# Kernel optimization log

Hardware: AMD Instinct MI355X
Metric: run time of the kernel (lower is better)

The kernel has to match this reference:

```python
import jax, jax.numpy as jnp
import numpy as np

H = 512      # hidden == embed (required: process-block LSTM consumes attention output of size hidden)
XY = 2
CITY_T = 100
BATCH = 512
INIT = 0.08  # uniform(-0.08, 0.08) weight init


def _unif(key, shape):
    return jax.random.uniform(key, shape, jnp.float32, minval=-INIT, maxval=INIT)


def lstm_cell(x, h, c, Wih, Whh, bih, bhh):
    # PyTorch gate order: i, f, g, o
    g = x @ Wih.T + h @ Whh.T + (bih + bhh)
    i, f, gg, o = jnp.split(g, 4, axis=-1)
    c_new = jax.nn.sigmoid(f) * c + jax.nn.sigmoid(i) * jnp.tanh(gg)
    h_new = jax.nn.sigmoid(o) * jnp.tanh(c_new)
    return h_new, c_new


def setup_inputs() -> dict:
    key = jax.random.key(0)
    ks = jax.random.split(key, 20)
    inp = {
        "x": jax.random.uniform(ks[0], (BATCH, CITY_T, XY), jnp.float32),      # city coords in [0,1)
        "dec_i1": jax.random.uniform(ks[1], (BATCH, H), jnp.float32),          # torch.rand(batch,1,hidden)
        "W_emb": _unif(ks[2], (H, XY)),
        "enc_Wih": _unif(ks[3], (4 * H, H)),
        "enc_Whh": _unif(ks[4], (4 * H, H)),
        "enc_bih": _unif(ks[5], (4 * H,)),
        "enc_bhh": _unif(ks[6], (4 * H,)),
        "dec_Wih": _unif(ks[7], (4 * H, H)),
        "dec_Whh": _unif(ks[8], (4 * H, H)),
        "dec_bih": _unif(ks[9], (4 * H,)),
        "dec_bhh": _unif(ks[10], (4 * H,)),
        "W_q": _unif(ks[11], (H, H)),
        "W_ref": _unif(ks[12], (H, H)),
        "v": _unif(ks[13], (1, H)),       # Vec: Linear(hidden,1,bias=False)
        "fc1": _unif(ks[14], (H, H)),
        "fc2": _unif(ks[15], (1, H)),
    }
    return inp


def reference(x, dec_i1, W_emb, enc_Wih, enc_Whh, enc_bih, enc_bhh,
              dec_Wih, dec_Whh, dec_bih, dec_bhh, W_q, W_ref, v, fc1, fc2):
    batch, city_t, _ = x.shape
    emb = x @ W_emb.T                                   # (b, c, H)

    # ---- Encoder LSTM (zero initial state) ----
    h0 = jnp.zeros((batch, H), emb.dtype)
    c0 = jnp.zeros((batch, H), emb.dtype)

    def enc_step(carry, xt):
        h, c = carry
        h, c = lstm_cell(xt, h, c, enc_Wih, enc_Whh, enc_bih, enc_bhh)
        return (h, c), h

    (hT, cT), enc_h = jax.lax.scan(enc_step, (h0, c0), jnp.swapaxes(emb, 0, 1))
    enc_h = jnp.swapaxes(enc_h, 0, 1)                   # (b, c, H)

    # W_ref(enc_h) is static across decode steps -> compute once
    u1 = enc_h @ W_ref.T                                # (b, c, H)

    # ---- Decoder: city_t steps of LSTM cell + Bahdanau attention ----
    def dec_step(carry, _):
        dec_i, h, c = carry
        h, c = lstm_cell(dec_i, h, c, dec_Wih, dec_Whh, dec_bih, dec_bhh)
        u2 = h @ W_q.T                                  # (b, H)
        u = jnp.tanh(u1 + u2[:, None, :]) @ v[0]        # (b, c)
        a = jax.nn.softmax(u, axis=1)
        d = jnp.einsum('bc,bch->bh', a, enc_h)          # glimpse (b, H)
        return (d, h, c), None

    (_, h_last, _), _ = jax.lax.scan(dec_step, (dec_i1, hT, cT), None, length=city_t)

    # final2FC: Linear->ReLU->Linear -> scalar per batch
    pred_l = jax.nn.relu(h_last @ fc1.T) @ fc2.T        # (b, 1)
    return pred_l[:, 0]
```

## Files before the change

### kernel.cpp

```cpp
#include <hip/hip_runtime.h>
#include <hip/hip_bf16.h>

#define H 512
#define TSTEPS 100
#define BATCH 512
#define KB 16
#define NBLK 256
#define NT 1024
#define NGRP 8
#define GBLK 32

typedef __attribute__((ext_vector_type(8))) short bf16x8;
typedef __attribute__((ext_vector_type(8))) unsigned short u16x8;
typedef __attribute__((ext_vector_type(4))) float f32x4;
typedef unsigned short u16;

__device__ __forceinline__ float bf2f(u16 u) {
    union { unsigned int i; float f; } z; z.i = ((unsigned int)u) << 16; return z.f;
}
__device__ __forceinline__ u16 f2bf(float f) {
    union { float f; unsigned int u; } z; z.f = f;
    unsigned int r = (z.u + 0x7fffu + ((z.u >> 16) & 1u)) >> 16;
    return (u16)r;
}
__device__ __forceinline__ float sigmoidf_(float x) { return 1.0f / (1.0f + __expf(-x)); }
__device__ __forceinline__ float ftanh(float x) {
    x = fminf(15.0f, fmaxf(-15.0f, x));
    float e = __expf(2.0f * x);
    return (e - 1.0f) / (e + 1.0f);
}
__device__ __forceinline__ f32x4 MF(bf16x8 a, bf16x8 b, f32x4 c) {
    return __builtin_amdgcn_mfma_f32_16x16x32_bf16(a, b, c, 0, 0, 0);
}

__device__ __forceinline__ size_t pidx(int m, int k) {
    int kb = k >> 5, kin = k & 31;
    int lane = (m & 15) + (((kin >> 2) & 3) << 4);
    int j = (kin & 3) + ((kin >> 4) << 2);
    return ((size_t)((m >> 4) * KB + kb) * 64 + lane) * 8 + j;
}

__device__ __forceinline__ void fbar(unsigned* flags, int grp, int bib, unsigned target) {
    __syncthreads();
    if (threadIdx.x < 64) {
        if (threadIdx.x == 0)
            __hip_atomic_store(&flags[(grp * 32 + bib) * 16], target,
                               __ATOMIC_RELEASE, __HIP_MEMORY_SCOPE_AGENT);
        const int l = threadIdx.x;
        bool done;
        do {
            unsigned v = target;
            if (l < 32)
                v = __hip_atomic_load(&flags[(grp * 32 + l) * 16],
                                      __ATOMIC_RELAXED, __HIP_MEMORY_SCOPE_AGENT);
            done = __all((int)(v >= target));
            if (!done) __builtin_amdgcn_s_sleep(1);
        } while (!done);
        __threadfence();
    }
    __syncthreads();
}

__global__ void prep_kernel(const float* __restrict__ W_emb, const float* __restrict__ enc_Wih,
                            const float* __restrict__ enc_bih, const float* __restrict__ enc_bhh,
                            const float* __restrict__ dec_bih, const float* __restrict__ dec_bhh,
                            float* __restrict__ Wc, float* __restrict__ bc, float* __restrict__ db) {
    int g = blockIdx.x * blockDim.x + threadIdx.x;
    if (g >= 4 * H) return;
    float s0 = 0.f, s1 = 0.f;
    for (int j = 0; j < H; ++j) {
        float w = enc_Wih[(size_t)g * H + j];
        s0 += w * W_emb[j * 2 + 0];
        s1 += w * W_emb[j * 2 + 1];
    }
    Wc[g * 2 + 0] = s0; Wc[g * 2 + 1] = s1;
    bc[g] = enc_bih[g] + enc_bhh[g];
    db[g] = dec_bih[g] + dec_bhh[g];
}

__global__ void pack_w(const float* __restrict__ W, u16* __restrict__ hi, u16* __restrict__ lo,
                       int total) {
    int idx = blockIdx.x * 256 + threadIdx.x;
    if (idx >= total) return;
    int m = idx >> 9, k = idx & 511;
    float v = W[idx];
    u16 h16 = f2bf(v);
    u16 l16 = f2bf(v - bf2f(h16));
    size_t p = pidx(m, k);
    hi[p] = h16; lo[p] = l16;
}

__global__ void zero4(float* __restrict__ p, int n) {
    int i = blockIdx.x * blockDim.x + threadIdx.x;
    if (i < n) p[i] = 0.f;
}

__global__ __launch_bounds__(NT, 1) void persist_enc(
    const float* __restrict__ x, const float* __restrict__ Wc, const float* __restrict__ bc,
    const u16* __restrict__ WeH, const u16* __restrict__ WeL,
    float* __restrict__ cbuf, u16* __restrict__ hbuf,
    u16* __restrict__ ench, unsigned* __restrict__ fE) {
    extern __shared__ char smem[];
    u16* wlds = (u16*)smem;
    float* exch = (float*)(smem + 131072);
    const int tid = threadIdx.x;
    const int lane = tid & 63;
    const int w = tid >> 6;
    const int q = w & 3, j = w >> 2;
    const int blk = blockIdx.x;
    const int grp = blk & 7, nni = blk >> 3;
    const size_t BHs = (size_t)BATCH * H;

    for (int c = 0; c < 8; ++c) {
        int cq = c >> 1, hl = c & 1;
        const u16x8* s8 = (const u16x8*)((hl ? WeL : WeH) + (size_t)((cq * 32 + nni) * KB) * 512);
        u16x8* d8 = (u16x8*)(wlds + c * 8192);
        for (int i = tid; i < 1024; i += NT) d8[i] = s8[i];
    }
    __syncthreads();

    for (int t = 0; t < TSTEPS; ++t) {
        const u16* Ah = hbuf + (size_t)(t & 1) * 2 * BHs;
        const u16* Al = Ah + BHs;
        u16* Hh = hbuf + (size_t)((t + 1) & 1) * 2 * BHs;
        u16* Hl = Hh + BHs;
        f32x4 acc = {};
#pragma unroll 4
        for (int kb = 0; kb < KB; ++kb) {
            bf16x8 bh = *(const bf16x8*)&wlds[((q * 2 + 0) * KB + kb) * 512 + lane * 8];
            bf16x8 bl = *(const bf16x8*)&wlds[((q * 2 + 1) * KB + kb) * 512 + lane * 8];
            size_t ab = ((size_t)((grp * 4 + j) * KB + kb) * 64 + lane) * 8;
            bf16x8 ah = *(const bf16x8*)&Ah[ab];
            bf16x8 al = *(const bf16x8*)&Al[ab];
            acc = MF(ah, bh, acc);
            acc = MF(ah, bl, acc);
            acc = MF(al, bh, acc);
        }
        const int col = lane & 15, rg = lane >> 4;
#pragma unroll
        for (int r = 0; r < 4; ++r)
            exch[(q * 64 + j * 16 + rg * 4 + r) * 16 + col] = acc[r];
        __syncthreads();
        {
            int lb = tid >> 4, cl = tid & 15;
            int b = grp * 64 + lb, n = nni * 16 + cl;
            float x0 = x[((size_t)b * TSTEPS + t) * 2 + 0];
            float x1 = x[((size_t)b * TSTEPS + t) * 2 + 1];
            float g[4];
#pragma unroll
            for (int qq = 0; qq < 4; ++qq)
                g[qq] = exch[(qq * 64 + lb) * 16 + cl] + bc[qq * H + n]
                      + x0 * Wc[(qq * H + n) * 2 + 0] + x1 * Wc[(qq * H + n) * 2 + 1];
            size_t ci = (size_t)b * H + n;
            float cn = sigmoidf_(g[1]) * cbuf[ci] + sigmoidf_(g[0]) * ftanh(g[2]);
            float hn = sigmoidf_(g[3]) * ftanh(cn);
            cbuf[ci] = cn;
            u16 hh = f2bf(hn), hl16 = f2bf(hn - bf2f(hh));
            size_t p = pidx(b, n);
            Hh[p] = hh; Hl[p] = hl16;
            ench[((size_t)b * TSTEPS + t) * H + n] = hh;
        }
        fbar(fE, grp, nni, (unsigned)(t + 1));
    }
}

__global__ __launch_bounds__(NT, 1) void persist_dec(
    const u16* __restrict__ WdiH, const u16* __restrict__ WdiL,
    const u16* __restrict__ WdhH, const u16* __restrict__ WdhL,
    const float* __restrict__ db,
    const u16* __restrict__ WqH, const u16* __restrict__ WqL,
    const u16* __restrict__ u1r, const u16* __restrict__ ench, const float* __restrict__ vv,
    float* __restrict__ cbuf, u16* __restrict__ hbuf,
    u16* __restrict__ dhi, u16* __restrict__ dlo,
    unsigned* __restrict__ fA, unsigned* __restrict__ fC) {
    extern __shared__ char smem[];
    u16* wlds = (u16*)smem;
    char* scratch = smem + 131072;
    float* exch  = (float*)scratch;
    float* u2row = (float*)scratch;
    float* ssc   = (float*)(scratch + 4096);
    float* ssm   = (float*)(scratch + 4928);
    f32x4* dacc  = (f32x4*)(scratch + 5760);
    const int tid = threadIdx.x;
    const int lane = tid & 63;
    const int w = tid >> 6;
    const int blk = blockIdx.x;
    const int grp = blk & 7, nni = blk >> 3;
    const size_t BHs = (size_t)BATCH * H;

    float vvr[8];
    {
        float4 v0 = *(const float4*)&vv[lane * 8];
        float4 v1 = *(const float4*)&vv[lane * 8 + 4];
        vvr[0] = v0.x; vvr[1] = v0.y; vvr[2] = v0.z; vvr[3] = v0.w;
        vvr[4] = v1.x; vvr[5] = v1.y; vvr[6] = v1.z; vvr[7] = v1.w;
    }

    for (int c = 0; c < 8; ++c) {
        int mat = c >> 2, cq = c & 3;
        const u16x8* s8 = (const u16x8*)((mat ? WdhH : WdiH) + (size_t)((cq * 32 + nni) * KB) * 512);
        u16x8* d8 = (u16x8*)(wlds + c * 8192);
        for (int i = tid; i < 1024; i += NT) d8[i] = s8[i];
    }
    __syncthreads();

    for (int s = 0; s < TSTEPS; ++s) {
        {
            const u16* hAh = hbuf + (size_t)(s & 1) * 2 * BHs;
            const u16* hAl = hAh + BHs;
            u16* Hh = hbuf + (size_t)((s + 1) & 1) * 2 * BHs;
            u16* Hl = Hh + BHs;
            const int q = w & 3, j = w >> 2;
            f32x4 acc = {};
#pragma unroll
            for (int ph = 0; ph < 2; ++ph) {
                const u16* Ah = ph ? hAh : dhi;
                const u16* Al = ph ? hAl : dlo;
                const u16* Wl = ph ? WdhL : WdiL;
#pragma unroll 4
                for (int kb = 0; kb < KB; ++kb) {
                    bf16x8 bh = *(const bf16x8*)&wlds[((ph * 4 + q) * KB + kb) * 512 + lane * 8];
                    bf16x8 bl = *(const bf16x8*)&Wl[((size_t)((q * 32 + nni) * KB + kb) * 64 + lane) * 8];
                    size_t ab = ((size_t)((grp * 4 + j) * KB + kb) * 64 + lane) * 8;
                    bf16x8 ah = *(const bf16x8*)&Ah[ab];
                    bf16x8 al = *(const bf16x8*)&Al[ab];
                    acc = MF(ah, bh, acc);
                    acc = MF(ah, bl, acc);
                    acc = MF(al, bh, acc);
                }
            }
            const int col = lane & 15, rg = lane >> 4;
#pragma unroll
            for (int r = 0; r < 4; ++r)
                exch[(q * 64 + j * 16 + rg * 4 + r) * 16 + col] = acc[r];
            __syncthreads();
            {
                int lb = tid >> 4, cl = tid & 15;
                int b = grp * 64 + lb, n = nni * 16 + cl;
                float g[4];
#pragma unroll
                for (int qq = 0; qq < 4; ++qq)
                    g[qq] = exch[(qq * 64 + lb) * 16 + cl] + db[qq * H + n];
                size_t ci = (size_t)b * H + n;
                float cn = sigmoidf_(g[1]) * cbuf[ci] + sigmoidf_(g[0]) * ftanh(g[2]);
                float hn = sigmoidf_(g[3]) * ftanh(cn);
                cbuf[ci] = cn;
                u16 hh = f2bf(hn), hl16 = f2bf(hn - bf2f(hh));
                size_t p = pidx(b, n);
                Hh[p] = hh; Hl[p] = hl16;
            }
        }
        if (s == TSTEPS - 1) break;
        fbar(fA, grp, nni, (unsigned)(s + 1));

        {
            const int r = tid >> 9;
            const int par = (tid >> 6) & 7;
            const int cnt = (par < 4) ? 13 : 12;
            const int brow = grp * 64 + 2 * nni + r;
            const u16* u1base = &u1r[(size_t)brow * TSTEPS * H + lane * 8];
            const u16* ehbase = &ench[(size_t)brow * TSTEPS * H + lane * 8];
            u16x8 evA[8];
#pragma unroll
            for (int u = 0; u < 8; ++u)
                evA[u] = *(const u16x8*)&ehbase[(size_t)(par + 8 * u) * H];

            {
                const u16* Ah = hbuf + (size_t)((s + 1) & 1) * 2 * BHs;
                const u16* Al = Ah + BHs;
                const int mf = grp * 4 + (nni >> 3);
                f32x4 acc[2] = {};
#pragma unroll 4
                for (int kb = 0; kb < KB; ++kb) {
                    size_t ab = ((size_t)(mf * KB + kb) * 64 + lane) * 8;
                    bf16x8 ah = *(const bf16x8*)&Ah[ab];
                    bf16x8 al = *(const bf16x8*)&Al[ab];
#pragma unroll
                    for (int f = 0; f < 2; ++f) {
                        int n16 = w * 2 + f;
                        size_t fb = ((size_t)(n16 * KB + kb) * 64 + lane) * 8;
                        bf16x8 bh = *(const bf16x8*)&WqH[fb];
                        bf16x8 bl = *(const bf16x8*)&WqL[fb];
                        acc[f] = MF(ah, bh, acc[f]);
                        acc[f] = MF(ah, bl, acc[f]);
                        acc[f] = MF(al, bh, acc[f]);
                    }
                }
                const int col = lane & 15, rg = lane >> 4;
                const int t0 = (nni & 7) * 2;
#pragma unroll
                for (int f = 0; f < 2; ++f)
#pragma unroll
                    for (int rr = 0; rr < 4; ++rr) {
                        int m = rg * 4 + rr;
                        int n = (w * 2 + f) * 16 + col;
                        if (m == t0)     u2row[n] = acc[f][rr];
                        if (m == t0 + 1) u2row[512 + n] = acc[f][rr];
                    }
            }
            __syncthreads();

            float u2v[8];
            {
                float4 a0 = *(const float4*)&u2row[r * 512 + lane * 8];
                float4 a1 = *(const float4*)&u2row[r * 512 + lane * 8 + 4];
                u2v[0] = a0.x; u2v[1] = a0.y; u2v[2] = a0.z; u2v[3] = a0.w;
                u2v[4] = a1.x; u2v[5] = a1.y; u2v[6] = a1.z; u2v[7] = a1.w;
            }
            for (int i0 = 0; i0 < 13; i0 += 5) {
                u16x8 uvv[5];
#pragma unroll
                for (int u = 0; u < 5; ++u) {
                    int i = i0 + u;
                    if (i < cnt)
                        uvv[u] = *(const u16x8*)&u1base[(size_t)(par + 8 * i) * H];
                }
#pragma unroll
                for (int u = 0; u < 5; ++u) {
                    int i = i0 + u;
                    if (i < cnt) {
                        float pp = 0.f;
#pragma unroll
                        for (int jj = 0; jj < 8; ++jj)
                            pp += vvr[jj] * ftanh(bf2f(uvv[u][jj]) + u2v[jj]);
#pragma unroll
                        for (int off = 32; off; off >>= 1) pp += __shfl_xor(pp, off);
                        if (lane == 0) ssc[r * 100 + par + 8 * i] = pp;
                    }
                }
            }
            __syncthreads();
            if (tid < 128) {
                int r2 = tid >> 6, ln = tid & 63;
                float s1 = ssc[r2 * 100 + ln];
                float s2 = (ln + 64 < 100) ? ssc[r2 * 100 + ln + 64] : -1e30f;
                float m = fmaxf(s1, s2);
#pragma unroll
                for (int off = 32; off; off >>= 1) m = fmaxf(m, __shfl_xor(m, off));
                float e1 = __expf(s1 - m);
                float e2 = (ln + 64 < 100) ? __expf(s2 - m) : 0.f;
                float sum = e1 + e2;
#pragma unroll
                for (int off = 32; off; off >>= 1) sum += __shfl_xor(sum, off);
                float inv = 1.f / sum;
                ssm[r2 * 100 + ln] = e1 * inv;
                if (ln + 64 < 100) ssm[r2 * 100 + ln + 64] = e2 * inv;
            }
            __syncthreads();
            float ga[8] = {};
#pragma unroll
            for (int u = 0; u < 8; ++u) {
                float a = ssm[r * 100 + par + 8 * u];
#pragma unroll
                for (int jj = 0; jj < 8; ++jj) ga[jj] += a * bf2f(evA[u][jj]);
            }
            {
                u16x8 evB[5];
#pragma unroll
                for (int u = 0; u < 5; ++u) {
                    int i = 8 + u;
                    if (i < cnt)
                        evB[u] = *(const u16x8*)&ehbase[(size_t)(par + 8 * i) * H];
                }
#pragma unroll
                for (int u = 0; u < 5; ++u) {
                    int i = 8 + u;
                    if (i < cnt) {
                        float a = ssm[r * 100 + par + 8 * i];
#pragma unroll
                        for (int jj = 0; jj < 8; ++jj) ga[jj] += a * bf2f(evB[u][jj]);
                    }
                }
            }
            f32x4 g0 = {ga[0], ga[1], ga[2], ga[3]};
            f32x4 g1 = {ga[4], ga[5], ga[6], ga[7]};
            if (par < 4) {
                dacc[(((par * 2 + r) * 64) + lane) * 2 + 0] = g0;
                dacc[(((par * 2 + r) * 64) + lane) * 2 + 1] = g1;
            }
            __syncthreads();
            if (par >= 4) {
                int slot = par - 4;
                f32x4 t0 = dacc[(((slot * 2 + r) * 64) + lane) * 2 + 0];
                f32x4 t1 = dacc[(((slot * 2 + r) * 64) + lane) * 2 + 1];
                dacc[(((slot * 2 + r) * 64) + lane) * 2 + 0] = t0 + g0;
                dacc[(((slot * 2 + r) * 64) + lane) * 2 + 1] = t1 + g1;
            }
            __syncthreads();
            if (tid < 128) {
                int r2 = tid >> 6, l = tid & 63;
                float fin[8];
#pragma unroll
                for (int jj = 0; jj < 8; ++jj) fin[jj] = 0.f;
#pragma unroll
                for (int sl = 0; sl < 4; ++sl) {
                    f32x4 d0 = dacc[(((sl * 2 + r2) * 64) + l) * 2 + 0];
                    f32x4 d1 = dacc[(((sl * 2 + r2) * 64) + l) * 2 + 1];
                    fin[0] += d0[0]; fin[1] += d0[1]; fin[2] += d0[2]; fin[3] += d0[3];
                    fin[4] += d1[0]; fin[5] += d1[1]; fin[6] += d1[2]; fin[7] += d1[3];
                }
                int b2 = grp * 64 + 2 * nni + r2;
                int h0 = l * 8;
#pragma unroll
                for (int qd = 0; qd < 2; ++qd) {
                    int k = h0 + 4 * qd;
                    size_t p = (((size_t)(b2 >> 4) * KB + (k >> 5)) * 64 + (b2 & 15)
                                + (((k >> 2) & 3) << 4)) * 8 + (((k >> 4) & 1) << 2);
                    float f0 = fin[4 * qd], f1 = fin[4 * qd + 1], f2 = fin[4 * qd + 2], f3 = fin[4 * qd + 3];
                    u16 a0 = f2bf(f0), a1 = f2bf(f1), a2 = f2bf(f2), a3 = f2bf(f3);
                    *(ushort4*)&dhi[p] = make_ushort4(a0, a1, a2, a3);
                    u16 c0 = f2bf(f0 - bf2f(a0)), c1 = f2bf(f1 - bf2f(a1));
                    u16 c2 = f2bf(f2 - bf2f(a2)), c3 = f2bf(f3 - bf2f(a3));
                    *(ushort4*)&dlo[p] = make_ushort4(c0, c1, c2, c3);
                }
            }
        }
        fbar(fC, grp, nni, (unsigned)(s + 1));
    }
}

__global__ __launch_bounds__(256) void gemm_u1(const u16* __restrict__ ench_row,
                                               const u16* __restrict__ Bh, const u16* __restrict__ Bl,
                                               u16* __restrict__ u1_row) {
    __shared__ u16 lds[2 * KB * 64 * 8];
    const int tid = threadIdx.x;
    const int m0 = blockIdx.x * 32;
    {
        int r = tid >> 3;
        int o = tid & 7;
#pragma unroll
        for (int p8 = 0; p8 < 8; ++p8) {
            int k0 = (o + 8 * p8) * 8;
            const u16* src = &ench_row[(size_t)(m0 + r) * H + k0];
            ushort4 v0 = *(const ushort4*)&src[0];
            ushort4 v1 = *(const ushort4*)&src[4];
            int kb = k0 >> 5, kin0 = k0 & 31;
            int g0 = (kin0 >> 2) & 3;
            int jo = (kin0 >> 4) << 2;
            u16* base = &lds[(size_t)(((r >> 4) * KB + kb) * 64) * 8];
            *(ushort4*)&base[((r & 15) + 16 * g0) * 8 + jo] = v0;
            *(ushort4*)&base[((r & 15) + 16 * (g0 + 1)) * 8 + jo] = v1;
        }
    }
    __syncthreads();
    const int lane = tid & 63;
    const int w = tid >> 6;
    const int mw = w & 1, nh = w >> 1;
    for (int nc = 0; nc < 16; ++nc) {
        int n16 = nh * 16 + nc;
        f32x4 acc = {};
#pragma unroll 4
        for (int kb = 0; kb < KB; ++kb) {
            bf16x8 a = *(const bf16x8*)&lds[((mw * KB + kb) * 64 + lane) * 8];
            size_t fb = ((size_t)(n16 * KB + kb) * 64 + lane) * 8;
            bf16x8 bh = *(const bf16x8*)&Bh[fb];
            bf16x8 bl = *(const bf16x8*)&Bl[fb];
            acc = MF(a, bh, acc);
            acc = MF(a, bl, acc);
        }
        const int col = lane & 15, rg = lane >> 4;
#pragma unroll
        for (int r = 0; r < 4; ++r) {
            size_t mrow = (size_t)m0 + mw * 16 + rg * 4 + r;
            u1_row[mrow * H + n16 * 16 + col] = f2bf(acc[r]);
        }
    }
}

__global__ __launch_bounds__(256) void final_kernel(const u16* __restrict__ hi,
                                                    const u16* __restrict__ lo,
                                                    const float* __restrict__ fc1,
                                                    const float* __restrict__ fc2,
                                                    float* __restrict__ out) {
    const int b = blockIdx.x;
    __shared__ float hsh[H];
    __shared__ float red[256];
    for (int i = threadIdx.x; i < H; i += 256) {
        size_t p = pidx(b, i);
        hsh[i] = bf2f(hi[p]) + bf2f(lo[p]);
    }
    __syncthreads();
    float total = 0.f;
    for (int n = threadIdx.x; n < H; n += 256) {
        float acc = 0.f;
        for (int j = 0; j < H; ++j) acc += fc1[(size_t)n * H + j] * hsh[j];
        total += fmaxf(acc, 0.f) * fc2[n];
    }
    red[threadIdx.x] = total;
    __syncthreads();
    for (int s = 128; s > 0; s >>= 1) {
        if (threadIdx.x < s) red[threadIdx.x] += red[threadIdx.x + s];
        __syncthreads();
    }
    if (threadIdx.x == 0) out[b] = red[0];
}

extern "C" void kernel_launch(void* const* d_in, const int* in_sizes, int n_in,
                              void* d_out, int out_size, void* d_ws, size_t ws_size,
                              hipStream_t stream) {
    (void)in_sizes; (void)n_in; (void)out_size;
    const float* x       = (const float*)d_in[0];
    const float* dec_i1  = (const float*)d_in[1];
    const float* W_emb   = (const float*)d_in[2];
    const float* enc_Wih = (const float*)d_in[3];
    const float* enc_Whh = (const float*)d_in[4];
    const float* enc_bih = (const float*)d_in[5];
    const float* enc_bhh = (const float*)d_in[6];
    const float* dec_Wih = (const float*)d_in[7];
    const float* dec_Whh = (const float*)d_in[8];
    const float* dec_bih = (const float*)d_in[9];
    const float* dec_bhh = (const float*)d_in[10];
    const float* W_q     = (const float*)d_in[11];
    const float* W_ref   = (const float*)d_in[12];
    const float* vv      = (const float*)d_in[13];
    const float* fc1     = (const float*)d_in[14];
    const float* fc2     = (const float*)d_in[15];
    float* out = (float*)d_out;

    const size_t BH = (size_t)BATCH * H;
    const size_t W4 = (size_t)4 * H * H;
    const size_t WS = (size_t)H * H;
    const size_t TBH = (size_t)TSTEPS * BATCH * H;

    unsigned* fA = (unsigned*)d_ws;
    unsigned* fC = fA + 4096;
    unsigned* fE = fC + 4096;
    float* c_  = (float*)(fE + 4096);
    u16* hbuf  = (u16*)(c_ + BH);
    float* Wc  = (float*)(hbuf + 4 * BH);
    float* bc  = Wc + 4 * H * 2;
    float* db  = bc + 4 * H;
    u16* dhi   = (u16*)(db + 4 * H);
    u16* dlo   = dhi + BH;
    u16* WeH   = dlo + BH;    u16* WeL  = WeH + W4;
    u16* WdiH  = WeL + W4;    u16* WdiL = WdiH + W4;
    u16* WdhH  = WdiL + W4;   u16* WdhL = WdhH + W4;
    u16* WqH   = WdhL + W4;   u16* WqL  = WqH + WS;
    u16* WrH   = WqL + WS;    u16* WrL  = WrH + WS;
    u16* ench  = WrL + WS;
    u16* u1r   = ench + TBH;

    size_t needed = (size_t)((char*)(u1r + TBH) - (char*)d_ws);
    if (ws_size < needed) return;

    const int ENC_SMEM = 131072 + 16384;
    const int DEC_SMEM = 131072 + 22528;
    (void)hipFuncSetAttribute((const void*)persist_enc, hipFuncAttributeMaxDynamicSharedMemorySize, ENC_SMEM);
    (void)hipFuncSetAttribute((const void*)persist_dec, hipFuncAttributeMaxDynamicSharedMemorySize, DEC_SMEM);

    prep_kernel<<<8, 256, 0, stream>>>(W_emb, enc_Wih, enc_bih, enc_bhh, dec_bih, dec_bhh, Wc, bc, db);
    pack_w<<<(int)(W4 / 256), 256, 0, stream>>>(enc_Whh, WeH, WeL, (int)W4);
    pack_w<<<(int)(W4 / 256), 256, 0, stream>>>(dec_Wih, WdiH, WdiL, (int)W4);
    pack_w<<<(int)(W4 / 256), 256, 0, stream>>>(dec_Whh, WdhH, WdhL, (int)W4);
    pack_w<<<(int)(WS / 256), 256, 0, stream>>>(W_q, WqH, WqL, (int)WS);
    pack_w<<<(int)(WS / 256), 256, 0, stream>>>(W_ref, WrH, WrL, (int)WS);
    pack_w<<<(int)(BH / 256), 256, 0, stream>>>(dec_i1, dhi, dlo, (int)BH);
    zero4<<<(int)((12288 + 3 * BH + 255) / 256), 256, 0, stream>>>((float*)d_ws, (int)(12288 + 3 * BH));

    persist_enc<<<NBLK, NT, ENC_SMEM, stream>>>(x, Wc, bc, WeH, WeL, c_, hbuf, ench, fE);
    gemm_u1<<<TSTEPS * BATCH / 32, 256, 0, stream>>>(ench, WrH, WrL, u1r);
    persist_dec<<<NBLK, NT, DEC_SMEM, stream>>>(WdiH, WdiL, WdhH, WdhL, db, WqH, WqL,
                                                u1r, ench, vv, c_, hbuf, dhi, dlo, fA, fC);
    final_kernel<<<BATCH, 256, 0, stream>>>(hbuf, hbuf + BH, fc1, fc2, out);
}
```

Baseline: 11.27 ms.

## Halve decoder block threads and keep u1 slice resident in registers

The persistent decoder now runs 512 threads per block instead of 1024. Each thread handles two gate tiles, four W_q output tiles and 25 cities of attention. The u1 slice for a thread's batch row and city range is loaded into registers once, before the decode loop, instead of being re-read from global memory every step. Encoder states for the glimpse are prefetched before the grid barrier, so their latency overlaps the wait, and one LDS reduction stage is dropped. In exchange, register pressure rises sharply (25+25 u16x8 vectors), which risks spills, and per-thread serial work doubles.

```diff
diff --git a/kernel.cpp b/kernel.cpp
--- a/kernel.cpp
+++ b/kernel.cpp
@@ -6,7 +6,8 @@
 #define BATCH 512
 #define KB 16
 #define NBLK 256
-#define NT 1024
+#define NTE 1024
+#define NT 512
 #define NGRP 8
 #define GBLK 32
 
@@ -95,7 +96,7 @@
     if (i < n) p[i] = 0.f;
 }
 
-__global__ __launch_bounds__(NT, 1) void persist_enc(
+__global__ __launch_bounds__(NTE, 1) void persist_enc(
     const float* __restrict__ x, const float* __restrict__ Wc, const float* __restrict__ bc,
     const u16* __restrict__ WeH, const u16* __restrict__ WeL,
     float* __restrict__ cbuf, u16* __restrict__ hbuf,
@@ -115,7 +116,7 @@
         int cq = c >> 1, hl = c & 1;
         const u16x8* s8 = (const u16x8*)((hl ? WeL : WeH) + (size_t)((cq * 32 + nni) * KB) * 512);
         u16x8* d8 = (u16x8*)(wlds + c * 8192);
-        for (int i = tid; i < 1024; i += NT) d8[i] = s8[i];
+        for (int i = tid; i < 1024; i += NTE) d8[i] = s8[i];
     }
     __syncthreads();
 
@@ -204,14 +205,26 @@
     }
     __syncthreads();
 
+    const int r_att = tid >> 8;
+    const int par = (tid >> 6) & 3;
+    const int ccb = par * 25;
+    const int brow = grp * 64 + 2 * nni + r_att;
+    const u16* u1base = &u1r[(size_t)brow * TSTEPS * H + lane * 8];
+    const u16* ehbase = &ench[(size_t)brow * TSTEPS * H + lane * 8];
+
+    u16x8 u1reg[25];
+#pragma unroll
+    for (int i = 0; i < 25; ++i)
+        u1reg[i] = *(const u16x8*)&u1base[(size_t)(ccb + i) * H];
+
     for (int s = 0; s < TSTEPS; ++s) {
         {
             const u16* hAh = hbuf + (size_t)(s & 1) * 2 * BHs;
             const u16* hAl = hAh + BHs;
             u16* Hh = hbuf + (size_t)((s + 1) & 1) * 2 * BHs;
             u16* Hl = Hh + BHs;
-            const int q = w & 3, j = w >> 2;
-            f32x4 acc = {};
+            const int q = w & 3, jh = w >> 2;
+            f32x4 acc[2] = {};
 #pragma unroll
             for (int ph = 0; ph < 2; ++ph) {
                 const u16* Ah = ph ? hAh : dhi;
@@ -221,21 +234,29 @@
                 for (int kb = 0; kb < KB; ++kb) {
                     bf16x8 bh = *(const bf16x8*)&wlds[((ph * 4 + q) * KB + kb) * 512 + lane * 8];
                     bf16x8 bl = *(const bf16x8*)&Wl[((size_t)((q * 32 + nni) * KB + kb) * 64 + lane) * 8];
-                    size_t ab = ((size_t)((grp * 4 + j) * KB + kb) * 64 + lane) * 8;
-                    bf16x8 ah = *(const bf16x8*)&Ah[ab];
-                    bf16x8 al = *(const bf16x8*)&Al[ab];
-                    acc = MF(ah, bh, acc);
-                    acc = MF(ah, bl, acc);
-                    acc = MF(al, bh, acc);
+#pragma unroll
+                    for (int jj = 0; jj < 2; ++jj) {
+                        int j = jh * 2 + jj;
+                        size_t ab = ((size_t)((grp * 4 + j) * KB + kb) * 64 + lane) * 8;
+                        bf16x8 ah = *(const bf16x8*)&Ah[ab];
+                        bf16x8 al = *(const bf16x8*)&Al[ab];
+                        acc[jj] = MF(ah, bh, acc[jj]);
+                        acc[jj] = MF(ah, bl, acc[jj]);
+                        acc[jj] = MF(al, bh, acc[jj]);
+                    }
                 }
             }
             const int col = lane & 15, rg = lane >> 4;
 #pragma unroll
-            for (int r = 0; r < 4; ++r)
-                exch[(q * 64 + j * 16 + rg * 4 + r) * 16 + col] = acc[r];
+            for (int jj = 0; jj < 2; ++jj)
+#pragma unroll
+                for (int r = 0; r < 4; ++r)
+                    exch[(q * 64 + (jh * 2 + jj) * 16 + rg * 4 + r) * 16 + col] = acc[jj][r];
             __syncthreads();
-            {
-                int lb = tid >> 4, cl = tid & 15;
+#pragma unroll
+            for (int k = 0; k < 2; ++k) {
+                int cell = k * NT + tid;
+                int lb = cell >> 4, cl = cell & 15;
                 int b = grp * 64 + lb, n = nni * 16 + cl;
                 float g[4];
 #pragma unroll
@@ -251,83 +272,65 @@
             }
         }
         if (s == TSTEPS - 1) break;
+
+        u16x8 ev[25];
+#pragma unroll
+        for (int u = 0; u < 25; ++u)
+            ev[u] = *(const u16x8*)&ehbase[(size_t)(ccb + u) * H];
+
         fbar(fA, grp, nni, (unsigned)(s + 1));
 
         {
-            const int r = tid >> 9;
-            const int par = (tid >> 6) & 7;
-            const int cnt = (par < 4) ? 13 : 12;
-            const int brow = grp * 64 + 2 * nni + r;
-            const u16* u1base = &u1r[(size_t)brow * TSTEPS * H + lane * 8];
-            const u16* ehbase = &ench[(size_t)brow * TSTEPS * H + lane * 8];
-            u16x8 evA[8];
-#pragma unroll
-            for (int u = 0; u < 8; ++u)
-                evA[u] = *(const u16x8*)&ehbase[(size_t)(par + 8 * u) * H];
-
-            {
-                const u16* Ah = hbuf + (size_t)((s + 1) & 1) * 2 * BHs;
-                const u16* Al = Ah + BHs;
-                const int mf = grp * 4 + (nni >> 3);
-                f32x4 acc[2] = {};
+            const u16* Ah = hbuf + (size_t)((s + 1) & 1) * 2 * BHs;
+            const u16* Al = Ah + BHs;
+            const int mf = grp * 4 + (nni >> 3);
+            f32x4 acc[4] = {};
 #pragma unroll 4
-                for (int kb = 0; kb < KB; ++kb) {
-                    size_t ab = ((size_t)(mf * KB + kb) * 64 + lane) * 8;
-                    bf16x8 ah = *(const bf16x8*)&Ah[ab];
-                    bf16x8 al = *(const bf16x8*)&Al[ab];
-#pragma unroll
-                    for (int f = 0; f < 2; ++f) {
-                        int n16 = w * 2 + f;
-                        size_t fb = ((size_t)(n16 * KB + kb) * 64 + lane) * 8;
-                        bf16x8 bh = *(const bf16x8*)&WqH[fb];
-                        bf16x8 bl = *(const bf16x8*)&WqL[fb];
-                        acc[f] = MF(ah, bh, acc[f]);
-                        acc[f] = MF(ah, bl, acc[f]);
-                        acc[f] = MF(al, bh, acc[f]);
-                    }
+            for (int kb = 0; kb < KB; ++kb) {
+                size_t ab = ((size_t)(mf * KB + kb) * 64 + lane) * 8;
+                bf16x8 ah = *(const bf16x8*)&Ah[ab];
+                bf16x8 al = *(const bf16x8*)&Al[ab];
+#pragma unroll
+                for (int f = 0; f < 4; ++f) {
+                    int n16 = w * 4 + f;
+                    size_t fb = ((size_t)(n16 * KB + kb) * 64 + lane) * 8;
+                    bf16x8 bh = *(const bf16x8*)&WqH[fb];
+                    bf16x8 bl = *(const bf16x8*)&WqL[fb];
+                    acc[f] = MF(ah, bh, acc[f]);
+                    acc[f] = MF(ah, bl, acc[f]);
+                    acc[f] = MF(al, bh, acc[f]);
                 }
-                const int col = lane & 15, rg = lane >> 4;
-                const int t0 = (nni & 7) * 2;
-#pragma unroll
-                for (int f = 0; f < 2; ++f)
-#pragma unroll
-                    for (int rr = 0; rr < 4; ++rr) {
-                        int m = rg * 4 + rr;
-                        int n = (w * 2 + f) * 16 + col;
-                        if (m == t0)     u2row[n] = acc[f][rr];
-                        if (m == t0 + 1) u2row[512 + n] = acc[f][rr];
-                    }
-            }
-            __syncthreads();
-
+            }
+            const int col = lane & 15, rg = lane >> 4;
+            const int t0 = (nni & 7) * 2;
+#pragma unroll
+            for (int f = 0; f < 4; ++f)
+#pragma unroll
+                for (int rr = 0; rr < 4; ++rr) {
+                    int m = rg * 4 + rr;
+                    int n = (w * 4 + f) * 16 + col;
+                    if (m == t0)     u2row[n] = acc[f][rr];
+                    if (m == t0 + 1) u2row[512 + n] = acc[f][rr];
+                }
+        }
+        __syncthreads();
+        {
             float u2v[8];
             {
-                float4 a0 = *(const float4*)&u2row[r * 512 + lane * 8];
-                float4 a1 = *(const float4*)&u2row[r * 512 + lane * 8 + 4];
+                float4 a0 = *(const float4*)&u2row[r_att * 512 + lane * 8];
+                float4 a1 = *(const float4*)&u2row[r_att * 512 + lane * 8 + 4];
                 u2v[0] = a0.x; u2v[1] = a0.y; u2v[2] = a0.z; u2v[3] = a0.w;
                 u2v[4] = a1.x; u2v[5] = a1.y; u2v[6] = a1.z; u2v[7] = a1.w;
             }
-            for (int i0 = 0; i0 < 13; i0 += 5) {
-                u16x8 uvv[5];
-#pragma unroll
-                for (int u = 0; u < 5; ++u) {
-                    int i = i0 + u;
-                    if (i < cnt)
-                        uvv[u] = *(const u16x8*)&u1base[(size_t)(par + 8 * i) * H];
-                }
-#pragma unroll
-                for (int u = 0; u < 5; ++u) {
-                    int i = i0 + u;
-                    if (i < cnt) {
-                        float pp = 0.f;
-#pragma unroll
-                        for (int jj = 0; jj < 8; ++jj)
-                            pp += vvr[jj] * ftanh(bf2f(uvv[u][jj]) + u2v[jj]);
-#pragma unroll
-                        for (int off = 32; off; off >>= 1) pp += __shfl_xor(pp, off);
-                        if (lane == 0) ssc[r * 100 + par + 8 * i] = pp;
-                    }
-                }
+#pragma unroll
+            for (int i = 0; i < 25; ++i) {
+                float pp = 0.f;
+#pragma unroll
+                for (int jj = 0; jj < 8; ++jj)
+                    pp += vvr[jj] * ftanh(bf2f(u1reg[i][jj]) + u2v[jj]);
+#pragma unroll
+                for (int off = 32; off; off >>= 1) pp += __shfl_xor(pp, off);
+                if (lane == 0) ssc[r_att * 100 + ccb + i] = pp;
             }
             __syncthreads();
             if (tid < 128) {
@@ -349,43 +352,15 @@
             __syncthreads();
             float ga[8] = {};
 #pragma unroll
-            for (int u = 0; u < 8; ++u) {
-                float a = ssm[r * 100 + par + 8 * u];
-#pragma unroll
-                for (int jj = 0; jj < 8; ++jj) ga[jj] += a * bf2f(evA[u][jj]);
-            }
-            {
-                u16x8 evB[5];
-#pragma unroll
-                for (int u = 0; u < 5; ++u) {
-                    int i = 8 + u;
-                    if (i < cnt)
-                        evB[u] = *(const u16x8*)&ehbase[(size_t)(par + 8 * i) * H];
-                }
-#pragma unroll
-                for (int u = 0; u < 5; ++u) {
-                    int i = 8 + u;
-                    if (i < cnt) {
-                        float a = ssm[r * 100 + par + 8 * i];
-#pragma unroll
-                        for (int jj = 0; jj < 8; ++jj) ga[jj] += a * bf2f(evB[u][jj]);
-                    }
-                }
+            for (int u = 0; u < 25; ++u) {
+                float a = ssm[r_att * 100 + ccb + u];
+#pragma unroll
+                for (int jj = 0; jj < 8; ++jj) ga[jj] += a * bf2f(ev[u][jj]);
             }
             f32x4 g0 = {ga[0], ga[1], ga[2], ga[3]};
             f32x4 g1 = {ga[4], ga[5], ga[6], ga[7]};
-            if (par < 4) {
-                dacc[(((par * 2 + r) * 64) + lane) * 2 + 0] = g0;
-                dacc[(((par * 2 + r) * 64) + lane) * 2 + 1] = g1;
-            }
-            __syncthreads();
-            if (par >= 4) {
-                int slot = par - 4;
-                f32x4 t0 = dacc[(((slot * 2 + r) * 64) + lane) * 2 + 0];
-                f32x4 t1 = dacc[(((slot * 2 + r) * 64) + lane) * 2 + 1];
-                dacc[(((slot * 2 + r) * 64) + lane) * 2 + 0] = t0 + g0;
-                dacc[(((slot * 2 + r) * 64) + lane) * 2 + 1] = t1 + g1;
-            }
+            dacc[(((par * 2 + r_att) * 64) + lane) * 2 + 0] = g0;
+            dacc[(((par * 2 + r_att) * 64) + lane) * 2 + 1] = g1;
             __syncthreads();
             if (tid < 128) {
                 int r2 = tid >> 6, l = tid & 63;
@@ -557,7 +532,7 @@
     pack_w<<<(int)(BH / 256), 256, 0, stream>>>(dec_i1, dhi, dlo, (int)BH);
     zero4<<<(int)((12288 + 3 * BH + 255) / 256), 256, 0, stream>>>((float*)d_ws, (int)(12288 + 3 * BH));
 
-    persist_enc<<<NBLK, NT, ENC_SMEM, stream>>>(x, Wc, bc, WeH, WeL, c_, hbuf, ench, fE);
+    persist_enc<<<NBLK, NTE, ENC_SMEM, stream>>>(x, Wc, bc, WeH, WeL, c_, hbuf, ench, fE);
     gemm_u1<<<TSTEPS * BATCH / 32, 256, 0, stream>>>(ench, WrH, WrL, u1r);
     persist_dec<<<NBLK, NT, DEC_SMEM, stream>>>(WdiH, WdiL, WdhH, WdhL, db, WqH, WqL,
                                                 u1r, ench, vv, c_, hbuf, dhi, dlo, fA, fC);
```

After: 17.28 ms. 53.3% more time.
